# Kernel tuning notes

Measured on AMD Instinct MI355X. Metric: run time of the kernel, lower is better.

Reference implementation:

```python
import jax, jax.numpy as jnp
import numpy as np

K = 3          # kernel_size
C = 3          # channels (hard-coded by the layer)
EPS = 0.1      # epsilon
B, H, W = 32, 512, 512


def setup_inputs() -> dict:
    key = jax.random.key(0)
    k1, k2, k3, k4 = jax.random.split(key, 4)
    x_t = jax.random.normal(k1, (B, H, W, C), jnp.float32)
    # TruncatedNormal(mean=10.0, stddev=0.05) per keras default stddev
    a = (10.0 + 0.05 * jax.random.normal(k2, (C, C))).astype(jnp.float32)
    b = (10.0 + 0.05 * jax.random.normal(k3, (C, C))).astype(jnp.float32)
    c = (10.0 + 0.05 * jax.random.normal(k4, (C, C))).astype(jnp.float32)
    bias = jnp.zeros((3,), jnp.float32)
    # channel_averaging_kernel: uniform kernel averaging over k*k window and 3 channels,
    # TF depthwise layout (K, K, C, 1)
    w = jnp.full((K, K, C, 1), 1.0 / (K * K * 3), jnp.float32)
    return {"x_t": x_t, "a": a, "b": b, "c": c, "bias": bias, "w": w}


def reference(x_t, a, b, c, bias, w):
    pad = (K - 1) // 2
    # toroidal (wrap) padding on spatial dims
    x_pad = jnp.pad(x_t, ((0, 0), (pad, pad), (pad, pad), (0, 0)), mode="wrap")
    # depthwise conv, VALID: TF kernel (K,K,C,1) -> lax HWIO (K,K,1,C) with groups=C
    rhs = jnp.transpose(w, (0, 1, 3, 2))  # (K, K, 1, C)
    x_hat = jax.lax.conv_general_dilated(
        x_pad, rhs, window_strides=(1, 1), padding="VALID",
        dimension_numbers=("NHWC", "HWIO", "NHWC"), feature_group_count=C)
    # per-pixel quadratic forms x_hat^T A x_hat for A in {a,b,c}, fused:
    # equals einsum('abci,abcj->abcij') then einsum('abcij,ij->abc') without
    # materializing the [B,H,W,3,3] outer product.
    M = jnp.stack([a, b, c], axis=0)                       # (3, C, C)
    delta = jnp.einsum("bhwi,kij,bhwj->bhwk", x_hat, M, x_hat) + bias  # (B,H,W,3)
    return x_t + EPS * delta
```

## Files before the change

kernel.cpp:

```cpp
#include <hip/hip_runtime.h>

#define HH 512
#define ROW4 384
#define RPW 2
#define EPS 0.1f

__global__ __launch_bounds__(256)
void gnllt_kernel(const float* __restrict__ xin,
                  const float* __restrict__ A,
                  const float* __restrict__ Bm,
                  const float* __restrict__ Cm,
                  const float* __restrict__ bias,
                  const float* __restrict__ wk,
                  float* __restrict__ outp)
{
    const int lane  = threadIdx.x & 63;
    const int wid   = (blockIdx.x << 2) | (threadIdx.x >> 6);
    const int strip = wid & 1;
    const int grp   = wid >> 1;
    const int img   = grp >> 8;
    const int h0    = (grp & 255) * RPW;

    const float wv = wk[0];
    const float qs = EPS * wv * wv;
    const float qa00 = qs*A[0],  qa11 = qs*A[4],  qa22 = qs*A[8];
    const float qa01 = qs*(A[1]+A[3]),  qa02 = qs*(A[2]+A[6]),  qa12 = qs*(A[5]+A[7]);
    const float qb00 = qs*Bm[0], qb11 = qs*Bm[4], qb22 = qs*Bm[8];
    const float qb01 = qs*(Bm[1]+Bm[3]), qb02 = qs*(Bm[2]+Bm[6]), qb12 = qs*(Bm[5]+Bm[7]);
    const float qc00 = qs*Cm[0], qc11 = qs*Cm[4], qc22 = qs*Cm[8];
    const float qc01 = qs*(Cm[1]+Cm[3]), qc02 = qs*(Cm[2]+Cm[6]), qc12 = qs*(Cm[5]+Cm[7]);
    const float bi0 = EPS*bias[0], bi1 = EPS*bias[1], bi2 = EPS*bias[2];

    const float4* x4 = (const float4*)xin;
    float4*       o4 = (float4*)outp;

    const int cb = strip * 192 + 3 * lane;
    int c[5];
    #pragma unroll
    for (int j = 0; j < 5; ++j) {
        int v = cb - 1 + j;
        if (v < 0)     v += ROW4;
        if (v >= ROW4) v -= ROW4;
        c[j] = v;
    }
    const size_t ib = (size_t)img * (HH * ROW4);

    float4 F[4][5];
    #pragma unroll
    for (int r = 0; r < 4; ++r) {
        const int hr = (h0 - 1 + r + HH) & (HH - 1);
        const float4* rp = x4 + ib + (size_t)hr * ROW4;
        #pragma unroll
        for (int j = 0; j < 5; ++j) F[r][j] = rp[c[j]];
    }

    float hs[4][12];
    float raw[2][12];
    #pragma unroll
    for (int r = 0; r < 4; ++r) {
        float g[20] = {F[r][0].x,F[r][0].y,F[r][0].z,F[r][0].w,
                       F[r][1].x,F[r][1].y,F[r][1].z,F[r][1].w,
                       F[r][2].x,F[r][2].y,F[r][2].z,F[r][2].w,
                       F[r][3].x,F[r][3].y,F[r][3].z,F[r][3].w,
                       F[r][4].x,F[r][4].y,F[r][4].z,F[r][4].w};
        #pragma unroll
        for (int q = 0; q < 12; ++q) hs[r][q] = g[1+q] + g[4+q] + g[7+q];
        if (r == 1 || r == 2) {
            #pragma unroll
            for (int q = 0; q < 12; ++q) raw[r-1][q] = g[4+q];
        }
    }

    #pragma unroll
    for (int i = 0; i < RPW; ++i) {
        const float* hm  = hs[i];
        const float* hc  = hs[i + 1];
        const float* hp  = hs[i + 2];
        const float* rw  = raw[i];

        float of[12];
        #pragma unroll
        for (int j = 0; j < 4; ++j) {
            const float s0 = hm[3*j+0] + hc[3*j+0] + hp[3*j+0];
            const float s1 = hm[3*j+1] + hc[3*j+1] + hp[3*j+1];
            const float s2 = hm[3*j+2] + hc[3*j+2] + hp[3*j+2];
            const float p00 = s0*s0, p11 = s1*s1, p22 = s2*s2;
            const float p01 = s0*s1, p02 = s0*s2, p12 = s1*s2;
            of[3*j+0] = rw[3*j+0] + bi0 + qa00*p00 + qa11*p11 + qa22*p22
                                        + qa01*p01 + qa02*p02 + qa12*p12;
            of[3*j+1] = rw[3*j+1] + bi1 + qb00*p00 + qb11*p11 + qb22*p22
                                        + qb01*p01 + qb02*p02 + qb12*p12;
            of[3*j+2] = rw[3*j+2] + bi2 + qc00*p00 + qc11*p11 + qc22*p22
                                        + qc01*p01 + qc02*p02 + qc12*p12;
        }

        float4* op = o4 + ib + (size_t)(h0 + i) * ROW4 + cb;
        op[0] = make_float4(of[0], of[1], of[2],  of[3]);
        op[1] = make_float4(of[4], of[5], of[6],  of[7]);
        op[2] = make_float4(of[8], of[9], of[10], of[11]);
    }
}

extern "C" void kernel_launch(void* const* d_in, const int* in_sizes, int n_in,
                              void* d_out, int out_size, void* d_ws, size_t ws_size,
                              hipStream_t stream) {
    const float* x    = (const float*)d_in[0];
    const float* A    = (const float*)d_in[1];
    const float* Bm   = (const float*)d_in[2];
    const float* Cm   = (const float*)d_in[3];
    const float* bias = (const float*)d_in[4];
    const float* wk   = (const float*)d_in[5];
    float* out = (float*)d_out;

    dim3 grid(4096);
    dim3 block(256);
    gnllt_kernel<<<grid, block, 0, stream>>>(x, A, Bm, Cm, bias, wk, out);
}
```

Before: 43.11 us.

## Stage input rows into LDS via async global_load_lds before stencil compute

```diff
diff --git a/kernel.cpp b/kernel.cpp
--- a/kernel.cpp
+++ b/kernel.cpp
@@ -1,9 +1,12 @@
 #include <hip/hip_runtime.h>
 
 #define HH 512
+#define ROWF 1536
 #define ROW4 384
-#define RPW 2
 #define EPS 0.1f
+
+typedef const __attribute__((address_space(1))) void* gas_t;
+typedef __attribute__((address_space(3))) void* las_t;
 
 __global__ __launch_bounds__(256)
 void gnllt_kernel(const float* __restrict__ xin,
@@ -14,12 +17,27 @@
                   const float* __restrict__ wk,
                   float* __restrict__ outp)
 {
-    const int lane  = threadIdx.x & 63;
-    const int wid   = (blockIdx.x << 2) | (threadIdx.x >> 6);
-    const int strip = wid & 1;
-    const int grp   = wid >> 1;
-    const int img   = grp >> 8;
-    const int h0    = (grp & 255) * RPW;
+    __shared__ float lds[6 * ROWF];
+
+    const int t    = threadIdx.x;
+    const int lane = t & 63;
+    const int w    = t >> 6;
+    const int blk  = blockIdx.x;
+    const int img  = blk >> 7;
+    const int r0   = (blk & 127) << 2;
+
+    const size_t ib = (size_t)img * (HH * ROW4);
+
+    #pragma unroll
+    for (int k = 0; k < 9; ++k) {
+        const int u    = 9 * w + k;
+        const int row  = u / 6;
+        const int col  = (u % 6) * 64;
+        const int srow = (r0 - 1 + row + HH) & (HH - 1);
+        const float* gp = xin + 4 * (ib + (size_t)srow * ROW4 + col + lane);
+        float* lp = lds + u * 256;
+        __builtin_amdgcn_global_load_lds((gas_t)gp, (las_t)lp, 16, 0, 0);
+    }
 
     const float wv = wk[0];
     const float qs = EPS * wv * wv;
@@ -31,52 +49,46 @@
     const float qc01 = qs*(Cm[1]+Cm[3]), qc02 = qs*(Cm[2]+Cm[6]), qc12 = qs*(Cm[5]+Cm[7]);
     const float bi0 = EPS*bias[0], bi1 = EPS*bias[1], bi2 = EPS*bias[2];
 
-    const float4* x4 = (const float4*)xin;
-    float4*       o4 = (float4*)outp;
+    __syncthreads();
 
-    const int cb = strip * 192 + 3 * lane;
+    const int g  = t & 127;
+    const int rb = (t >> 7) << 1;
+
     int c[5];
     #pragma unroll
     for (int j = 0; j < 5; ++j) {
-        int v = cb - 1 + j;
+        int v = 3 * g - 1 + j;
         if (v < 0)     v += ROW4;
         if (v >= ROW4) v -= ROW4;
         c[j] = v;
     }
-    const size_t ib = (size_t)img * (HH * ROW4);
 
-    float4 F[4][5];
+    float hsv[4][12];
+    float raw[2][12];
+
     #pragma unroll
-    for (int r = 0; r < 4; ++r) {
-        const int hr = (h0 - 1 + r + HH) & (HH - 1);
-        const float4* rp = x4 + ib + (size_t)hr * ROW4;
+    for (int s = 0; s < 4; ++s) {
+        const float4* lr = (const float4*)(lds + (rb + s) * ROWF);
+        const float4 F0 = lr[c[0]], F1 = lr[c[1]], F2 = lr[c[2]],
+                     F3 = lr[c[3]], F4 = lr[c[4]];
+        const float gg[20] = {F0.x,F0.y,F0.z,F0.w, F1.x,F1.y,F1.z,F1.w,
+                              F2.x,F2.y,F2.z,F2.w, F3.x,F3.y,F3.z,F3.w,
+                              F4.x,F4.y,F4.z,F4.w};
         #pragma unroll
-        for (int j = 0; j < 5; ++j) F[r][j] = rp[c[j]];
-    }
-
-    float hs[4][12];
-    float raw[2][12];
-    #pragma unroll
-    for (int r = 0; r < 4; ++r) {
-        float g[20] = {F[r][0].x,F[r][0].y,F[r][0].z,F[r][0].w,
-                       F[r][1].x,F[r][1].y,F[r][1].z,F[r][1].w,
-                       F[r][2].x,F[r][2].y,F[r][2].z,F[r][2].w,
-                       F[r][3].x,F[r][3].y,F[r][3].z,F[r][3].w,
-                       F[r][4].x,F[r][4].y,F[r][4].z,F[r][4].w};
-        #pragma unroll
-        for (int q = 0; q < 12; ++q) hs[r][q] = g[1+q] + g[4+q] + g[7+q];
-        if (r == 1 || r == 2) {
+        for (int q = 0; q < 12; ++q) hsv[s][q] = gg[1+q] + gg[4+q] + gg[7+q];
+        if (s == 1 || s == 2) {
             #pragma unroll
-            for (int q = 0; q < 12; ++q) raw[r-1][q] = g[4+q];
+            for (int q = 0; q < 12; ++q) raw[s-1][q] = gg[4+q];
         }
     }
 
+    float4* o4 = (float4*)outp;
     #pragma unroll
-    for (int i = 0; i < RPW; ++i) {
-        const float* hm  = hs[i];
-        const float* hc  = hs[i + 1];
-        const float* hp  = hs[i + 2];
-        const float* rw  = raw[i];
+    for (int k = 0; k < 2; ++k) {
+        const float* hm = hsv[k];
+        const float* hc = hsv[k + 1];
+        const float* hp = hsv[k + 2];
+        const float* rw = raw[k];
 
         float of[12];
         #pragma unroll
@@ -94,7 +106,7 @@
                                         + qc01*p01 + qc02*p02 + qc12*p12;
         }
 
-        float4* op = o4 + ib + (size_t)(h0 + i) * ROW4 + cb;
+        float4* op = o4 + ib + (size_t)(r0 + rb + k) * ROW4 + 3 * g;
         op[0] = make_float4(of[0], of[1], of[2],  of[3]);
         op[1] = make_float4(of[4], of[5], of[6],  of[7]);
         op[2] = make_float4(of[8], of[9], of[10], of[11]);
```

Result: slower. 44.43 us (+3.1%).
